# Kernel tuning notes

Measured on AMD Instinct MI355X. Metric: run time of the kernel, lower is better.

The kernel has to match this reference:

```python
import jax, jax.numpy as jnp
import numpy as np

TINY = 1e-15
K_CURV = -1.0
NEG_K = 1.0
SQRT_NEG_K = 1.0
B, D, OUT = 16384, 1024, 4096


def setup_inputs() -> dict:
    key = jax.random.key(0)
    k1, k2, k3 = jax.random.split(key, 3)
    x = jax.random.normal(k1, (B, D), dtype=jnp.float32)
    # PVManifoldMLR.reset_parameters: z ~ N(0, 0.01), r ~ U(-0.001, 0.001)
    z = 0.01 * jax.random.normal(k2, (OUT, D), dtype=jnp.float32)
    r = jax.random.uniform(k3, (OUT, 1), dtype=jnp.float32, minval=-0.001, maxval=0.001)
    bias = jnp.zeros((OUT,), dtype=jnp.float32)
    return {"x": x, "z": z, "r": r, "bias": bias}


def _mlr(x, z, r):
    # PVManifoldMLR.forward (PVNN Thm 5.2 hyperplane distances)
    z_norm = jnp.clip(jnp.linalg.norm(z, axis=-1, keepdims=True), TINY, None)  # [OUT,1]
    sr = jnp.clip(SQRT_NEG_K * r[:, 0], -15.0, 15.0)                            # [OUT]
    cosh_sr = jnp.cosh(sr)
    sinh_sr = jnp.sinh(sr)
    xz = x @ z.T                                                                 # [B,OUT]
    term_A = cosh_sr[None, :] * xz
    x_sq = jnp.sum(x * x, axis=-1, keepdims=True)                                # [B,1]
    beta_inv = jnp.sqrt(1.0 - K_CURV * x_sq)                                     # sqrt(1+|K|x^2)
    term_B = (sinh_sr[None, :] / SQRT_NEG_K) * z_norm.T * beta_inv
    factor_C = SQRT_NEG_K / z_norm.T
    argument = jnp.clip(factor_C * (term_A - term_B), -1e6, 1e6)
    scale = z_norm.T / SQRT_NEG_K
    return scale * jnp.arcsinh(argument)                                         # [B,OUT]


def reference(x, z, r, bias):
    # PVFC: v = MLR(x) + bias; inner_act='none'; y = (1/sqrt(-K)) * sinh(sqrt(-K) * v)
    v = _mlr(x, z, r) + bias[None, :]
    return (1.0 / SQRT_NEG_K) * jnp.sinh(SQRT_NEG_K * v)
```

## Files before the change

### kernel.cpp

```cpp
#include <hip/hip_runtime.h>
#include <stdint.h>
#include <math.h>

#define B_ROWS 16384
#define D_DIM  1024
#define OUT_N  4096

typedef __bf16 bf16x8 __attribute__((ext_vector_type(8)));
typedef float  f32x4  __attribute__((ext_vector_type(4)));

__device__ __forceinline__ unsigned short f2bf(float f) {
  union { float f; uint32_t u; } v; v.f = f;
  uint32_t u = v.u;
  u += 0x7FFFu + ((u >> 16) & 1u);
  return (unsigned short)(u >> 16);
}

__global__ void prep_kernel(const float* __restrict__ x,
                            const float* __restrict__ z,
                            const float* __restrict__ r,
                            unsigned short* __restrict__ xbf,
                            unsigned short* __restrict__ zbf,
                            float* __restrict__ beta,
                            float4* __restrict__ zp) {
  const int b = blockIdx.x;
  const int t = threadIdx.x;
  __shared__ float ws4[4];
  if (b < B_ROWS) {
    const int row = b;
    const float4 v = reinterpret_cast<const float4*>(x + (size_t)row * D_DIM)[t];
    float ssq = v.x * v.x + v.y * v.y + v.z * v.z + v.w * v.w;
    ushort4 h;
    h.x = f2bf(v.x); h.y = f2bf(v.y); h.z = f2bf(v.z); h.w = f2bf(v.w);
    reinterpret_cast<ushort4*>(xbf + (size_t)row * D_DIM)[t] = h;
#pragma unroll
    for (int off = 32; off > 0; off >>= 1) ssq += __shfl_down(ssq, off);
    if ((t & 63) == 0) ws4[t >> 6] = ssq;
    __syncthreads();
    if (t == 0) {
      float s = ws4[0] + ws4[1] + ws4[2] + ws4[3];
      beta[row] = sqrtf(1.0f + s);
    }
  } else {
    const int row = b - B_ROWS;
    const float4 v = reinterpret_cast<const float4*>(z + (size_t)row * D_DIM)[t];
    float ssq = v.x * v.x + v.y * v.y + v.z * v.z + v.w * v.w;
    ushort4 h;
    h.x = f2bf(v.x); h.y = f2bf(v.y); h.z = f2bf(v.z); h.w = f2bf(v.w);
    reinterpret_cast<ushort4*>(zbf + (size_t)row * D_DIM)[t] = h;
#pragma unroll
    for (int off = 32; off > 0; off >>= 1) ssq += __shfl_down(ssq, off);
    if ((t & 63) == 0) ws4[t >> 6] = ssq;
    __syncthreads();
    if (t == 0) {
      float s = ws4[0] + ws4[1] + ws4[2] + ws4[3];
      float zn = fmaxf(sqrtf(s), 1e-15f);
      float sr = fminf(fmaxf(r[row], -15.0f), 15.0f);
      float ch = coshf(sr), sh = sinhf(sr);
      zp[row] = make_float4(ch, sh * zn, zn, 1.0f / zn);
    }
  }
}


__device__ __forceinline__ void gload_lds16(const void* g, void* l) {
  __builtin_amdgcn_global_load_lds((__attribute__((address_space(1))) void*)g,
                                   (__attribute__((address_space(3))) void*)l,
                                   16, 0, 0);
}

#define FENCE() asm volatile("" ::: "memory")
#define BARRIER() do { FENCE(); __builtin_amdgcn_s_barrier(); FENCE(); } while (0)
#define WAITVM4() asm volatile("s_waitcnt vmcnt(4)" ::: "memory")
#define WAITVM0() asm volatile("s_waitcnt vmcnt(0)" ::: "memory")

__device__ __forceinline__ float epi(float arg, float zn, float bia) {
  const float LN2   = 0.6931471805599453f;
  const float LOG2E = 1.4426950408889634f;
  float ax = fabsf(arg);
  float s  = __builtin_amdgcn_sqrtf(fmaf(ax, ax, 1.0f));
  float as = __builtin_amdgcn_logf(ax + s) * LN2;
  float v  = fmaf(zn, copysignf(as, arg), bia);
  float e  = __builtin_amdgcn_exp2f(v * LOG2E);
  return 0.5f * (e - __builtin_amdgcn_rcpf(e));
}

__device__ __forceinline__ void stage_half(const unsigned short* __restrict__ src,
                                           int grow0, int k0,
                                           unsigned short* ldsbase,
                                           int wave, int lane) {
#pragma unroll
  for (int j = 0; j < 2; ++j) {
    const int c = wave * 2 + j;
    const int r = c * 8 + (lane >> 3);
    const int col8 = (lane & 7) ^ (lane >> 3);
    gload_lds16(src + (size_t)(grow0 + r) * D_DIM + k0 + col8 * 8,
                ldsbase + c * 512);
  }
}

__device__ __forceinline__ void load_a(bf16x8 a[4][2], const unsigned short* Ab,
                                       int qm, int lrow, int lgrp) {
  const int key = lrow & 7;
#pragma unroll
  for (int mi = 0; mi < 4; ++mi)
#pragma unroll
    for (int ks = 0; ks < 2; ++ks)
      a[mi][ks] = *reinterpret_cast<const bf16x8*>(
          &Ab[(qm * 64 + mi * 16 + lrow) * 64 + ((ks * 4 + lgrp) ^ key) * 8]);
}

__device__ __forceinline__ void load_b(bf16x8 b[2][2], const unsigned short* Bb,
                                       int qn, int lrow, int lgrp) {
  const int key = lrow & 7;
#pragma unroll
  for (int ni = 0; ni < 2; ++ni)
#pragma unroll
    for (int ks = 0; ks < 2; ++ks)
      b[ni][ks] = *reinterpret_cast<const bf16x8*>(
          &Bb[(qn * 32 + ni * 16 + lrow) * 64 + ((ks * 4 + lgrp) ^ key) * 8]);
}

__device__ __forceinline__ void mma_quad(f32x4 acc[8][4], const bf16x8 a[4][2],
                                         const bf16x8 b[2][2], int qm, int qn) {
  __builtin_amdgcn_s_setprio(1);
#pragma unroll
  for (int mi = 0; mi < 4; ++mi)
#pragma unroll
    for (int ni = 0; ni < 2; ++ni)
#pragma unroll
      for (int ks = 0; ks < 2; ++ks)
        acc[qm * 4 + mi][qn * 2 + ni] = __builtin_amdgcn_mfma_f32_16x16x32_bf16(
            a[mi][ks], b[ni][ks], acc[qm * 4 + mi][qn * 2 + ni], 0, 0, 0);
  __builtin_amdgcn_s_setprio(0);
}

__global__ __launch_bounds__(512) void gemm_fused(
    const unsigned short* __restrict__ xbf,
    const unsigned short* __restrict__ zbf,
    const float* __restrict__ beta,
    const float4* __restrict__ zp,
    const float* __restrict__ bias,
    float* __restrict__ out) {
  __shared__ unsigned short lds[65536];

  const int t = threadIdx.x;
  const int lane = t & 63;
  const int wave = t >> 6;
  const int wm = wave >> 2;
  const int wn = wave & 3;
  const int lrow = lane & 15;
  const int lgrp = lane >> 4;

  const int bid = blockIdx.x;
  const int xcd = bid & 7;
  const int j   = bid >> 3;
  const int m0 = (xcd * 8 + (j & 7)) * 256;
  const int n0 = (j >> 3) * 256;

  unsigned short* A0 = lds + wm * 8192;
  unsigned short* A1 = lds + 32768 + wm * 8192;
  unsigned short* B0 = lds + 16384 + (wn >> 1) * 8192 + (wn & 1) * 4096;
  unsigned short* B1 = B0 + 32768;

  f32x4 acc[8][4] = {};
  bf16x8 a[4][2], b0[2][2], b1[2][2];

  stage_half(xbf, m0,       0, lds,                 wave, lane);
  stage_half(xbf, m0 + 128, 0, lds + 8192,          wave, lane);
  stage_half(zbf, n0,       0, lds + 16384,         wave, lane);
  stage_half(zbf, n0 + 128, 0, lds + 16384 + 8192,  wave, lane);
  stage_half(zbf, n0,      64, lds + 32768 + 16384,        wave, lane);
  stage_half(zbf, n0 + 128,64, lds + 32768 + 16384 + 8192, wave, lane);
  WAITVM4();
  BARRIER();

#pragma unroll 1
  for (int i = 0; i < 8; ++i) {
    const int kA1 = (2 * i + 1) * 64;
    const int kT2 = (2 * i + 2) * 64;
    const int kT3 = (2 * i + 3) * 64;
    const bool more = (i < 7);

    load_a(a, A0, 0, lrow, lgrp);
    load_b(b0, B0, 0, lrow, lgrp);
    stage_half(xbf, m0, kA1, lds + 32768, wave, lane);
    BARRIER();
    mma_quad(acc, a, b0, 0, 0);
    BARRIER();
    load_b(b1, B0, 1, lrow, lgrp);
    stage_half(xbf, m0 + 128, kA1, lds + 32768 + 8192, wave, lane);
    BARRIER();
    mma_quad(acc, a, b1, 0, 1);
    BARRIER();
    load_a(a, A0, 1, lrow, lgrp);
    if (more) stage_half(zbf, n0, kT2, lds + 16384, wave, lane);
    BARRIER();
    mma_quad(acc, a, b0, 1, 0);
    BARRIER();
    if (more) stage_half(zbf, n0 + 128, kT2, lds + 16384 + 8192, wave, lane);
    BARRIER();
    mma_quad(acc, a, b1, 1, 1);
    if (more) { WAITVM4(); } else { WAITVM0(); }
    BARRIER();

    load_a(a, A1, 0, lrow, lgrp);
    load_b(b0, B1, 0, lrow, lgrp);
    if (more) stage_half(xbf, m0, kT2, lds, wave, lane);
    BARRIER();
    mma_quad(acc, a, b0, 0, 0);
    BARRIER();
    load_b(b1, B1, 1, lrow, lgrp);
    if (more) stage_half(xbf, m0 + 128, kT2, lds + 8192, wave, lane);
    BARRIER();
    mma_quad(acc, a, b1, 0, 1);
    BARRIER();
    load_a(a, A1, 1, lrow, lgrp);
    if (more) stage_half(zbf, n0, kT3, lds + 32768 + 16384, wave, lane);
    BARRIER();
    mma_quad(acc, a, b0, 1, 0);
    BARRIER();
    if (more) stage_half(zbf, n0 + 128, kT3, lds + 32768 + 16384 + 8192, wave, lane);
    BARRIER();
    mma_quad(acc, a, b1, 1, 1);
    if (more) WAITVM4();
    BARRIER();
  }

  float4 pq[4];
  float biaq[4];
#pragma unroll
  for (int ni = 0; ni < 4; ++ni) {
    const int o = n0 + wn * 64 + ni * 16 + lrow;
    pq[ni] = zp[o];
    biaq[ni] = bias[o];
  }
  const int ocol0 = n0 + wn * 64 + lrow;

#pragma unroll
  for (int mi = 0; mi < 8; ++mi) {
    const int r0 = m0 + wm * 128 + mi * 16 + lgrp * 4;
    float bt[4];
#pragma unroll
    for (int jj = 0; jj < 4; ++jj) bt[jj] = beta[r0 + jj];
#pragma unroll
    for (int jj = 0; jj < 4; ++jj) {
      const size_t rowbase = (size_t)(r0 + jj) * OUT_N + ocol0;
#pragma unroll
      for (int ni = 0; ni < 4; ++ni) {
        float arg = (pq[ni].x * acc[mi][ni][jj] - pq[ni].y * bt[jj]) * pq[ni].w;
        arg = fminf(fmaxf(arg, -1e6f), 1e6f);
        out[rowbase + ni * 16] = epi(arg, pq[ni].z, biaq[ni]);
      }
    }
  }
}


extern "C" void kernel_launch(void* const* d_in, const int* in_sizes, int n_in,
                              void* d_out, int out_size, void* d_ws, size_t ws_size,
                              hipStream_t stream) {
  const float* x    = (const float*)d_in[0];
  const float* z    = (const float*)d_in[1];
  const float* r    = (const float*)d_in[2];
  const float* bias = (const float*)d_in[3];
  float* out = (float*)d_out;

  char* ws = (char*)d_ws;
  unsigned short* xbf = (unsigned short*)ws;
  unsigned short* zbf = (unsigned short*)(ws + (size_t)32 * 1024 * 1024);
  float* beta = (float*)(ws + (size_t)40 * 1024 * 1024);
  float4* zp  = (float4*)(ws + (size_t)40 * 1024 * 1024 + 64 * 1024);

  prep_kernel<<<dim3(B_ROWS + OUT_N), dim3(256), 0, stream>>>(x, z, r, xbf, zbf, beta, zp);
  gemm_fused<<<dim3((B_ROWS / 256) * (OUT_N / 256)), dim3(512), 0, stream>>>(
      xbf, zbf, beta, zp, bias, out);
}
```

Before: 197.8 us.

## Switch GEMM to 32x32x16 MFMA tiles and fold epilogue constants into prep

```diff
diff --git a/kernel.cpp b/kernel.cpp
--- a/kernel.cpp
+++ b/kernel.cpp
@@ -7,7 +7,7 @@
 #define OUT_N  4096
 
 typedef __bf16 bf16x8 __attribute__((ext_vector_type(8)));
-typedef float  f32x4  __attribute__((ext_vector_type(4)));
+typedef float  f32x16 __attribute__((ext_vector_type(16)));
 
 __device__ __forceinline__ unsigned short f2bf(float f) {
   union { float f; uint32_t u; } v; v.f = f;
@@ -19,6 +19,7 @@
 __global__ void prep_kernel(const float* __restrict__ x,
                             const float* __restrict__ z,
                             const float* __restrict__ r,
+                            const float* __restrict__ bias,
                             unsigned short* __restrict__ xbf,
                             unsigned short* __restrict__ zbf,
                             float* __restrict__ beta,
@@ -57,7 +58,8 @@
       float zn = fmaxf(sqrtf(s), 1e-15f);
       float sr = fminf(fmaxf(r[row], -15.0f), 15.0f);
       float ch = coshf(sr), sh = sinhf(sr);
-      zp[row] = make_float4(ch, sh * zn, zn, 1.0f / zn);
+      const float LOG2E = 1.4426950408889634f;
+      zp[row] = make_float4(ch / zn, sh, zn, bias[row] * LOG2E);
     }
   }
 }
@@ -73,17 +75,6 @@
 #define BARRIER() do { FENCE(); __builtin_amdgcn_s_barrier(); FENCE(); } while (0)
 #define WAITVM4() asm volatile("s_waitcnt vmcnt(4)" ::: "memory")
 #define WAITVM0() asm volatile("s_waitcnt vmcnt(0)" ::: "memory")
-
-__device__ __forceinline__ float epi(float arg, float zn, float bia) {
-  const float LN2   = 0.6931471805599453f;
-  const float LOG2E = 1.4426950408889634f;
-  float ax = fabsf(arg);
-  float s  = __builtin_amdgcn_sqrtf(fmaf(ax, ax, 1.0f));
-  float as = __builtin_amdgcn_logf(ax + s) * LN2;
-  float v  = fmaf(zn, copysignf(as, arg), bia);
-  float e  = __builtin_amdgcn_exp2f(v * LOG2E);
-  return 0.5f * (e - __builtin_amdgcn_rcpf(e));
-}
 
 __device__ __forceinline__ void stage_half(const unsigned short* __restrict__ src,
                                            int grow0, int k0,
@@ -99,39 +90,41 @@
   }
 }
 
-__device__ __forceinline__ void load_a(bf16x8 a[4][2], const unsigned short* Ab,
-                                       int qm, int lrow, int lgrp) {
-  const int key = lrow & 7;
-#pragma unroll
-  for (int mi = 0; mi < 4; ++mi)
-#pragma unroll
-    for (int ks = 0; ks < 2; ++ks)
+__device__ __forceinline__ void load_a32(bf16x8 a[2][4], const unsigned short* Ab,
+                                         int qm, int lane) {
+  const int rl  = lane & 31;
+  const int kh  = lane >> 5;
+  const int key = lane & 7;
+#pragma unroll
+  for (int mi = 0; mi < 2; ++mi) {
+    const int row = qm * 64 + mi * 32 + rl;
+#pragma unroll
+    for (int ks = 0; ks < 4; ++ks)
       a[mi][ks] = *reinterpret_cast<const bf16x8*>(
-          &Ab[(qm * 64 + mi * 16 + lrow) * 64 + ((ks * 4 + lgrp) ^ key) * 8]);
-}
-
-__device__ __forceinline__ void load_b(bf16x8 b[2][2], const unsigned short* Bb,
-                                       int qn, int lrow, int lgrp) {
-  const int key = lrow & 7;
-#pragma unroll
-  for (int ni = 0; ni < 2; ++ni)
-#pragma unroll
-    for (int ks = 0; ks < 2; ++ks)
-      b[ni][ks] = *reinterpret_cast<const bf16x8*>(
-          &Bb[(qn * 32 + ni * 16 + lrow) * 64 + ((ks * 4 + lgrp) ^ key) * 8]);
-}
-
-__device__ __forceinline__ void mma_quad(f32x4 acc[8][4], const bf16x8 a[4][2],
-                                         const bf16x8 b[2][2], int qm, int qn) {
+          &Ab[row * 64 + ((ks * 2 + kh) ^ key) * 8]);
+  }
+}
+
+__device__ __forceinline__ void load_b32(bf16x8 b[4], const unsigned short* Bb,
+                                         int qn, int lane) {
+  const int row = qn * 32 + (lane & 31);
+  const int kh  = lane >> 5;
+  const int key = lane & 7;
+#pragma unroll
+  for (int ks = 0; ks < 4; ++ks)
+    b[ks] = *reinterpret_cast<const bf16x8*>(
+        &Bb[row * 64 + ((ks * 2 + kh) ^ key) * 8]);
+}
+
+__device__ __forceinline__ void mma_quad32(f32x16 acc[4][2], const bf16x8 a[2][4],
+                                           const bf16x8 b[4], int qm, int qn) {
   __builtin_amdgcn_s_setprio(1);
 #pragma unroll
-  for (int mi = 0; mi < 4; ++mi)
-#pragma unroll
-    for (int ni = 0; ni < 2; ++ni)
-#pragma unroll
-      for (int ks = 0; ks < 2; ++ks)
-        acc[qm * 4 + mi][qn * 2 + ni] = __builtin_amdgcn_mfma_f32_16x16x32_bf16(
-            a[mi][ks], b[ni][ks], acc[qm * 4 + mi][qn * 2 + ni], 0, 0, 0);
+  for (int ks = 0; ks < 4; ++ks)
+#pragma unroll
+    for (int mi = 0; mi < 2; ++mi)
+      acc[qm * 2 + mi][qn] = __builtin_amdgcn_mfma_f32_32x32x16_bf16(
+          a[mi][ks], b[ks], acc[qm * 2 + mi][qn], 0, 0, 0);
   __builtin_amdgcn_s_setprio(0);
 }
 
@@ -140,7 +133,6 @@
     const unsigned short* __restrict__ zbf,
     const float* __restrict__ beta,
     const float4* __restrict__ zp,
-    const float* __restrict__ bias,
     float* __restrict__ out) {
   __shared__ unsigned short lds[65536];
 
@@ -149,8 +141,6 @@
   const int wave = t >> 6;
   const int wm = wave >> 2;
   const int wn = wave & 3;
-  const int lrow = lane & 15;
-  const int lgrp = lane >> 4;
 
   const int bid = blockIdx.x;
   const int xcd = bid & 7;
@@ -163,8 +153,8 @@
   unsigned short* B0 = lds + 16384 + (wn >> 1) * 8192 + (wn & 1) * 4096;
   unsigned short* B1 = B0 + 32768;
 
-  f32x4 acc[8][4] = {};
-  bf16x8 a[4][2], b0[2][2], b1[2][2];
+  f32x16 acc[4][2] = {};
+  bf16x8 a[2][4], b0[4], b1[4];
 
   stage_half(xbf, m0,       0, lds,                 wave, lane);
   stage_half(xbf, m0 + 128, 0, lds + 8192,          wave, lane);
@@ -182,75 +172,79 @@
     const int kT3 = (2 * i + 3) * 64;
     const bool more = (i < 7);
 
-    load_a(a, A0, 0, lrow, lgrp);
-    load_b(b0, B0, 0, lrow, lgrp);
+    load_a32(a, A0, 0, lane);
+    load_b32(b0, B0, 0, lane);
     stage_half(xbf, m0, kA1, lds + 32768, wave, lane);
     BARRIER();
-    mma_quad(acc, a, b0, 0, 0);
-    BARRIER();
-    load_b(b1, B0, 1, lrow, lgrp);
+    mma_quad32(acc, a, b0, 0, 0);
+    BARRIER();
+    load_b32(b1, B0, 1, lane);
     stage_half(xbf, m0 + 128, kA1, lds + 32768 + 8192, wave, lane);
     BARRIER();
-    mma_quad(acc, a, b1, 0, 1);
-    BARRIER();
-    load_a(a, A0, 1, lrow, lgrp);
+    mma_quad32(acc, a, b1, 0, 1);
+    BARRIER();
+    load_a32(a, A0, 1, lane);
     if (more) stage_half(zbf, n0, kT2, lds + 16384, wave, lane);
     BARRIER();
-    mma_quad(acc, a, b0, 1, 0);
+    mma_quad32(acc, a, b0, 1, 0);
     BARRIER();
     if (more) stage_half(zbf, n0 + 128, kT2, lds + 16384 + 8192, wave, lane);
     BARRIER();
-    mma_quad(acc, a, b1, 1, 1);
+    mma_quad32(acc, a, b1, 1, 1);
     if (more) { WAITVM4(); } else { WAITVM0(); }
     BARRIER();
 
-    load_a(a, A1, 0, lrow, lgrp);
-    load_b(b0, B1, 0, lrow, lgrp);
+    load_a32(a, A1, 0, lane);
+    load_b32(b0, B1, 0, lane);
     if (more) stage_half(xbf, m0, kT2, lds, wave, lane);
     BARRIER();
-    mma_quad(acc, a, b0, 0, 0);
-    BARRIER();
-    load_b(b1, B1, 1, lrow, lgrp);
+    mma_quad32(acc, a, b0, 0, 0);
+    BARRIER();
+    load_b32(b1, B1, 1, lane);
     if (more) stage_half(xbf, m0 + 128, kT2, lds + 8192, wave, lane);
     BARRIER();
-    mma_quad(acc, a, b1, 0, 1);
-    BARRIER();
-    load_a(a, A1, 1, lrow, lgrp);
+    mma_quad32(acc, a, b1, 0, 1);
+    BARRIER();
+    load_a32(a, A1, 1, lane);
     if (more) stage_half(zbf, n0, kT3, lds + 32768 + 16384, wave, lane);
     BARRIER();
-    mma_quad(acc, a, b0, 1, 0);
+    mma_quad32(acc, a, b0, 1, 0);
     BARRIER();
     if (more) stage_half(zbf, n0 + 128, kT3, lds + 32768 + 16384 + 8192, wave, lane);
     BARRIER();
-    mma_quad(acc, a, b1, 1, 1);
+    mma_quad32(acc, a, b1, 1, 1);
     if (more) WAITVM4();
     BARRIER();
   }
 
-  float4 pq[4];
-  float biaq[4];
-#pragma unroll
-  for (int ni = 0; ni < 4; ++ni) {
-    const int o = n0 + wn * 64 + ni * 16 + lrow;
-    pq[ni] = zp[o];
-    biaq[ni] = bias[o];
-  }
-  const int ocol0 = n0 + wn * 64 + lrow;
-
-#pragma unroll
-  for (int mi = 0; mi < 8; ++mi) {
-    const int r0 = m0 + wm * 128 + mi * 16 + lgrp * 4;
-    float bt[4];
-#pragma unroll
-    for (int jj = 0; jj < 4; ++jj) bt[jj] = beta[r0 + jj];
-#pragma unroll
-    for (int jj = 0; jj < 4; ++jj) {
-      const size_t rowbase = (size_t)(r0 + jj) * OUT_N + ocol0;
-#pragma unroll
-      for (int ni = 0; ni < 4; ++ni) {
-        float arg = (pq[ni].x * acc[mi][ni][jj] - pq[ni].y * bt[jj]) * pq[ni].w;
-        arg = fminf(fmaxf(arg, -1e6f), 1e6f);
-        out[rowbase + ni * 16] = epi(arg, pq[ni].z, biaq[ni]);
+  const int hi   = lane >> 5;
+  const int col0 = n0 + wn * 64 + (lane & 31);
+  float4 pq[2];
+#pragma unroll
+  for (int ni = 0; ni < 2; ++ni) pq[ni] = zp[col0 + ni * 32];
+
+#pragma unroll
+  for (int Mi = 0; Mi < 4; ++Mi) {
+#pragma unroll
+    for (int q = 0; q < 4; ++q) {
+      const int r0 = m0 + wm * 128 + Mi * 32 + q * 8 + hi * 4;
+      const float4 b4 = *reinterpret_cast<const float4*>(&beta[r0]);
+      const float btv[4] = {b4.x, b4.y, b4.z, b4.w};
+#pragma unroll
+      for (int jj = 0; jj < 4; ++jj) {
+        const size_t rowbase = (size_t)(r0 + jj) * OUT_N + col0;
+#pragma unroll
+        for (int ni = 0; ni < 2; ++ni) {
+          float acv = acc[Mi][ni][q * 4 + jj];
+          float arg = fmaf(pq[ni].x, acv, -(pq[ni].y * btv[jj]));
+          float ax  = fminf(fabsf(arg), 1e6f);
+          float s   = __builtin_amdgcn_sqrtf(fmaf(ax, ax, 1.0f));
+          float tl  = __builtin_amdgcn_logf(ax + s);
+          float zs  = copysignf(pq[ni].z, arg);
+          float e   = __builtin_amdgcn_exp2f(fmaf(zs, tl, pq[ni].w));
+          float rc  = __builtin_amdgcn_rcpf(e);
+          out[rowbase + ni * 32] = fmaf(-0.5f, rc, 0.5f * e);
+        }
       }
     }
   }
@@ -272,7 +266,7 @@
   float* beta = (float*)(ws + (size_t)40 * 1024 * 1024);
   float4* zp  = (float4*)(ws + (size_t)40 * 1024 * 1024 + 64 * 1024);
 
-  prep_kernel<<<dim3(B_ROWS + OUT_N), dim3(256), 0, stream>>>(x, z, r, xbf, zbf, beta, zp);
+  prep_kernel<<<dim3(B_ROWS + OUT_N), dim3(256), 0, stream>>>(x, z, r, bias, xbf, zbf, beta, zp);
   gemm_fused<<<dim3((B_ROWS / 256) * (OUT_N / 256)), dim3(512), 0, stream>>>(
-      xbf, zbf, beta, zp, bias, out);
-}
+      xbf, zbf, beta, zp, out);
+}
```

Result: slower. 215.4 us (+8.9%).
